# Optimization experiments

Hardware: AMD Instinct MI355X
Metric: run time of the kernel (lower is better)

The kernel has to match this reference:

```python
import jax, jax.numpy as jnp
import numpy as np

TEMPERATURE = 1.0


def setup_inputs() -> dict:
    key = jax.random.key(0)
    k1, k2, k3, k4, k5 = jax.random.split(key, 5)
    B, D, Da, Dv = 8192, 128, 64, 64
    return {
        "a_features": jax.random.normal(k1, (B, D), dtype=jnp.float32),
        "v_features": jax.random.normal(k2, (B, D), dtype=jnp.float32),
        "audio_only_indices": jax.random.randint(k3, (Da,), 0, D, dtype=jnp.int64),
        "image_only_indices": jax.random.randint(k4, (Dv,), 0, D, dtype=jnp.int64),
        "labels": jax.random.randint(k5, (B,), 0, 10, dtype=jnp.int64),
    }


def reference(a_features, v_features, audio_only_indices, image_only_indices, labels):
    # Gather modality-specific feature subspaces: [B, Da] / [B, Dv]
    audio_only = a_features[:, audio_only_indices]          # a-features, audio dims
    image_audio_only = v_features[:, audio_only_indices]    # v-features, audio dims
    image_only = v_features[:, image_only_indices]          # v-features, image dims
    audio_image_only = a_features[:, image_only_indices]    # a-features, image dims

    # Per original: the dot-product partner is detached (stop_gradient).
    # v_loss_i = -log( exp(<v_i, a_i>/T) / sum_j exp(<v_i, a_j>/T) )
    #          = logsumexp_j(S_v[i, j]) - S_v[i, i]
    S_v = jnp.matmul(image_audio_only,
                     jax.lax.stop_gradient(audio_only).T) / TEMPERATURE  # [B, B]
    S_a = jnp.matmul(audio_image_only,
                     jax.lax.stop_gradient(image_only).T) / TEMPERATURE  # [B, B]

    v_loss = jnp.mean(jax.nn.logsumexp(S_v, axis=1) - jnp.diagonal(S_v))
    a_loss = jnp.mean(jax.nn.logsumexp(S_a, axis=1) - jnp.diagonal(S_a))
    return v_loss + a_loss
```

## Files before the change

### kernel.cpp

```cpp
#include <hip/hip_runtime.h>
#include <hip/hip_bf16.h>

typedef __attribute__((ext_vector_type(8))) short bf16x8;
typedef __attribute__((ext_vector_type(4))) float f32x4;

#define BN 8192
#define DF 128
#define DG 64
static constexpr float L2E = 1.44269504088896340736f;
static constexpr float LN2 = 0.69314718055994530942f;

__device__ __forceinline__ size_t frag_off(int row, int d) {
  int tile = row >> 4, m = row & 15;
  int half = d >> 5, q = (d >> 3) & 3, c = d & 7;
  return (size_t)tile * 1024 + (size_t)half * 512 + (size_t)(q * 16 + m) * 8 + c;
}

__global__ __launch_bounds__(256) void gather_k(
    const float* __restrict__ a, const float* __restrict__ v,
    const int* __restrict__ aidx, const int* __restrict__ iidx,
    __hip_bfloat16* __restrict__ Xv, __hip_bfloat16* __restrict__ Ya,
    __hip_bfloat16* __restrict__ Xa, __hip_bfloat16* __restrict__ Yv,
    float* __restrict__ diag, float* __restrict__ rowsum,
    float* __restrict__ out) {
  int tid = threadIdx.x;
  int gid = blockIdx.x * 256 + tid;
  if (gid < 2 * BN) rowsum[gid] = 0.f;
  if (gid == 0) out[0] = 0.f;

  int lane = tid & 63;
  int row  = blockIdx.x * 4 + (tid >> 6);
  int ka = aidx[lane];
  int ki = iidx[lane];

  float2 a2 = ((const float2*)(a + (size_t)row * DF))[lane];
  float2 v2 = ((const float2*)(v + (size_t)row * DF))[lane];

  float axa = __shfl(a2.x, ka >> 1), aya = __shfl(a2.y, ka >> 1);
  float vxa = __shfl(v2.x, ka >> 1), vya = __shfl(v2.y, ka >> 1);
  float axi = __shfl(a2.x, ki >> 1), ayi = __shfl(a2.y, ki >> 1);
  float vxi = __shfl(v2.x, ki >> 1), vyi = __shfl(v2.y, ki >> 1);
  float aa = (ka & 1) ? aya : axa;
  float va = (ka & 1) ? vya : vxa;
  float ai = (ki & 1) ? ayi : axi;
  float vi = (ki & 1) ? vyi : vxi;

  size_t fo = frag_off(row, lane);
  Xv[fo] = __float2bfloat16(va * L2E);
  Ya[fo] = __float2bfloat16(aa);
  Xa[fo] = __float2bfloat16(ai * L2E);
  Yv[fo] = __float2bfloat16(vi);

  float dv = va * aa;
  float da = ai * vi;
#pragma unroll
  for (int off = 32; off >= 1; off >>= 1) {
    dv += __shfl_xor(dv, off);
    da += __shfl_xor(da, off);
  }
  if (lane == 0) {
    diag[row]      = dv;
    diag[BN + row] = da;
  }
}

__global__ __launch_bounds__(256, 8) void lse_main(
    const unsigned short* __restrict__ Xv, const unsigned short* __restrict__ Ya,
    const unsigned short* __restrict__ Xa, const unsigned short* __restrict__ Yv,
    float* __restrict__ rowsum) {
  const unsigned short* X;
  const unsigned short* Y;
  float* rs;
  if (blockIdx.z == 0) { X = Xv; Y = Ya; rs = rowsum; }
  else                 { X = Xa; Y = Yv; rs = rowsum + BN; }

  int tid  = threadIdx.x;
  int lane = tid & 63;
  int m = lane & 15;
  int q = lane >> 4;
  int row0 = blockIdx.x * 128 + (tid >> 6) * 32;

  bf16x8 af[2][2];
#pragma unroll
  for (int t = 0; t < 2; ++t) {
    const unsigned short* p =
        X + (size_t)(row0 / 16 + t) * 1024 + (size_t)lane * 8;
    af[t][0] = *(const bf16x8*)p;
    af[t][1] = *(const bf16x8*)(p + 512);
  }

  f32x4 part[2] = {};
  const f32x4 zero = {0.f, 0.f, 0.f, 0.f};

  const unsigned short* bbase =
      Y + (size_t)(blockIdx.y * 32) * 1024 + (size_t)lane * 8;
  bf16x8 b0 = *(const bf16x8*)bbase;
  bf16x8 b1 = *(const bf16x8*)(bbase + 512);

#define LSE_BODY(B0, B1)                                                      \
  {                                                                           \
    _Pragma("unroll") for (int t = 0; t < 2; ++t) {                           \
      f32x4 c =                                                               \
          __builtin_amdgcn_mfma_f32_16x16x32_bf16(af[t][0], B0, zero, 0, 0, 0); \
      c = __builtin_amdgcn_mfma_f32_16x16x32_bf16(af[t][1], B1, c, 0, 0, 0);  \
      f32x4 e;                                                                \
      e[0] = __builtin_amdgcn_exp2f(c[0]);                                    \
      e[1] = __builtin_amdgcn_exp2f(c[1]);                                    \
      e[2] = __builtin_amdgcn_exp2f(c[2]);                                    \
      e[3] = __builtin_amdgcn_exp2f(c[3]);                                    \
      part[t] += e;                                                           \
    }                                                                         \
  }

  for (int jt = 0; jt < 31; ++jt) {
    const unsigned short* np = bbase + (size_t)(jt + 1) * 1024;
    bf16x8 n0 = *(const bf16x8*)np;
    bf16x8 n1 = *(const bf16x8*)(np + 512);
    LSE_BODY(b0, b1)
    b0 = n0;
    b1 = n1;
  }
  LSE_BODY(b0, b1)
#undef LSE_BODY

#pragma unroll
  for (int off = 1; off < 16; off <<= 1) {
#pragma unroll
    for (int t = 0; t < 2; ++t) {
#pragma unroll
      for (int r = 0; r < 4; ++r)
        part[t][r] += __shfl_xor(part[t][r], off);
    }
  }
  if (m == 0) {
#pragma unroll
    for (int t = 0; t < 2; ++t)
#pragma unroll
      for (int r = 0; r < 4; ++r)
        atomicAdd(&rs[row0 + t * 16 + q * 4 + r], part[t][r]);
  }
}

__global__ __launch_bounds__(256) void finalize_k(
    const float* __restrict__ rowsum, const float* __restrict__ diag,
    float* __restrict__ out) {
  int i = blockIdx.x * 256 + threadIdx.x;
  float local = LN2 * __builtin_amdgcn_logf(rowsum[i]) - diag[i];
#pragma unroll
  for (int off = 32; off >= 1; off >>= 1) local += __shfl_xor(local, off);
  __shared__ float red[4];
  int wave = threadIdx.x >> 6;
  if ((threadIdx.x & 63) == 0) red[wave] = local;
  __syncthreads();
  if (threadIdx.x == 0) {
    float bs = red[0] + red[1] + red[2] + red[3];
    atomicAdd(out, bs * (1.f / (float)BN));
  }
}

extern "C" void kernel_launch(void* const* d_in, const int* in_sizes, int n_in,
                              void* d_out, int out_size, void* d_ws, size_t ws_size,
                              hipStream_t stream) {
  const float* a   = (const float*)d_in[0];
  const float* v   = (const float*)d_in[1];
  const int* aidx  = (const int*)d_in[2];
  const int* iidx  = (const int*)d_in[3];

  char* ws = (char*)d_ws;
  const size_t MB = 1024 * 1024;
  __hip_bfloat16* Xv = (__hip_bfloat16*)(ws + 0 * MB);
  __hip_bfloat16* Ya = (__hip_bfloat16*)(ws + 1 * MB);
  __hip_bfloat16* Xa = (__hip_bfloat16*)(ws + 2 * MB);
  __hip_bfloat16* Yv = (__hip_bfloat16*)(ws + 3 * MB);
  float* diag   = (float*)(ws + 4 * MB);
  float* rowsum = (float*)(ws + 4 * MB + 64 * 1024);

  gather_k<<<BN / 4, 256, 0, stream>>>(a, v, aidx, iidx, Xv, Ya, Xa, Yv,
                                       diag, rowsum, (float*)d_out);
  lse_main<<<dim3(BN / 128, 16, 2), 256, 0, stream>>>(
      (const unsigned short*)Xv, (const unsigned short*)Ya,
      (const unsigned short*)Xa, (const unsigned short*)Yv, rowsum);
  finalize_k<<<64, 256, 0, stream>>>(rowsum, diag, (float*)d_out);
}
```

Before: 93.17 us.

## Switch LSE kernel to 32x32x16 MFMA with ping-pong exp/MFMA overlap

Repacks the bf16 gathered operands into a 32-row fragment layout and has each wave compute 32x32 tiles with mfma_f32_32x32x16_bf16 chains. Two accumulators alternate so one tile's exp2 and accumulation overlap the next tile's MFMA chain, with setprio raised around the MFMAs. The column split is halved (grid y from 16 to 8), so each block covers 1024 columns and there are fewer atomics. The 16-wide accumulators need more registers, so occupancy is capped at 4 blocks per SM instead of 8.

```diff
diff --git a/kernel.cpp b/kernel.cpp
--- a/kernel.cpp
+++ b/kernel.cpp
@@ -3,6 +3,7 @@
 
 typedef __attribute__((ext_vector_type(8))) short bf16x8;
 typedef __attribute__((ext_vector_type(4))) float f32x4;
+typedef __attribute__((ext_vector_type(16))) float f32x16;
 
 #define BN 8192
 #define DF 128
@@ -10,10 +11,11 @@
 static constexpr float L2E = 1.44269504088896340736f;
 static constexpr float LN2 = 0.69314718055994530942f;
 
-__device__ __forceinline__ size_t frag_off(int row, int d) {
-  int tile = row >> 4, m = row & 15;
-  int half = d >> 5, q = (d >> 3) & 3, c = d & 7;
-  return (size_t)tile * 1024 + (size_t)half * 512 + (size_t)(q * 16 + m) * 8 + c;
+__device__ __forceinline__ size_t frag_off32(int row, int d) {
+  int tile = row >> 5;
+  int kk = d >> 4, khi = (d >> 3) & 1, c = d & 7;
+  return (size_t)tile * 2048 + (size_t)kk * 512 +
+         (size_t)(khi * 32 + (row & 31)) * 8 + c;
 }
 
 __global__ __launch_bounds__(256) void gather_k(
@@ -45,7 +47,7 @@
   float ai = (ki & 1) ? ayi : axi;
   float vi = (ki & 1) ? vyi : vxi;
 
-  size_t fo = frag_off(row, lane);
+  size_t fo = frag_off32(row, lane);
   Xv[fo] = __float2bfloat16(va * L2E);
   Ya[fo] = __float2bfloat16(aa);
   Xa[fo] = __float2bfloat16(ai * L2E);
@@ -64,7 +66,7 @@
   }
 }
 
-__global__ __launch_bounds__(256, 8) void lse_main(
+__global__ __launch_bounds__(256, 4) void lse_main(
     const unsigned short* __restrict__ Xv, const unsigned short* __restrict__ Ya,
     const unsigned short* __restrict__ Xa, const unsigned short* __restrict__ Yv,
     float* __restrict__ rowsum) {
@@ -76,68 +78,77 @@
 
   int tid  = threadIdx.x;
   int lane = tid & 63;
-  int m = lane & 15;
-  int q = lane >> 4;
   int row0 = blockIdx.x * 128 + (tid >> 6) * 32;
 
-  bf16x8 af[2][2];
+  const unsigned short* ap =
+      X + (size_t)(row0 >> 5) * 2048 + (size_t)lane * 8;
+  bf16x8 a[4];
 #pragma unroll
-  for (int t = 0; t < 2; ++t) {
-    const unsigned short* p =
-        X + (size_t)(row0 / 16 + t) * 1024 + (size_t)lane * 8;
-    af[t][0] = *(const bf16x8*)p;
-    af[t][1] = *(const bf16x8*)(p + 512);
+  for (int kk = 0; kk < 4; ++kk) a[kk] = *(const bf16x8*)(ap + kk * 512);
+
+  const unsigned short* bbase =
+      Y + (size_t)(blockIdx.y * 32) * 2048 + (size_t)lane * 8;
+
+  const f32x16 zero16 = {};
+  f32x16 part = {};
+  bf16x8 b[4];
+
+#define LOADB(T)                                                              \
+  {                                                                           \
+    const unsigned short* p = bbase + (size_t)(T) * 2048;                     \
+    b[0] = *(const bf16x8*)p;                                                 \
+    b[1] = *(const bf16x8*)(p + 512);                                         \
+    b[2] = *(const bf16x8*)(p + 1024);                                        \
+    b[3] = *(const bf16x8*)(p + 1536);                                        \
+  }
+#define CHAIN(DST)                                                            \
+  {                                                                           \
+    __builtin_amdgcn_s_setprio(1);                                            \
+    DST = __builtin_amdgcn_mfma_f32_32x32x16_bf16(a[0], b[0], zero16, 0, 0, 0); \
+    DST = __builtin_amdgcn_mfma_f32_32x32x16_bf16(a[1], b[1], DST, 0, 0, 0);  \
+    DST = __builtin_amdgcn_mfma_f32_32x32x16_bf16(a[2], b[2], DST, 0, 0, 0);  \
+    DST = __builtin_amdgcn_mfma_f32_32x32x16_bf16(a[3], b[3], DST, 0, 0, 0);  \
+    __builtin_amdgcn_s_setprio(0);                                            \
+  }
+#define EXPACC(C)                                                             \
+  {                                                                           \
+    _Pragma("unroll") for (int r = 0; r < 16; ++r)                            \
+        part[r] += __builtin_amdgcn_exp2f(C[r]);                              \
   }
 
-  f32x4 part[2] = {};
-  const f32x4 zero = {0.f, 0.f, 0.f, 0.f};
-
-  const unsigned short* bbase =
-      Y + (size_t)(blockIdx.y * 32) * 1024 + (size_t)lane * 8;
-  bf16x8 b0 = *(const bf16x8*)bbase;
-  bf16x8 b1 = *(const bf16x8*)(bbase + 512);
-
-#define LSE_BODY(B0, B1)                                                      \
-  {                                                                           \
-    _Pragma("unroll") for (int t = 0; t < 2; ++t) {                           \
-      f32x4 c =                                                               \
-          __builtin_amdgcn_mfma_f32_16x16x32_bf16(af[t][0], B0, zero, 0, 0, 0); \
-      c = __builtin_amdgcn_mfma_f32_16x16x32_bf16(af[t][1], B1, c, 0, 0, 0);  \
-      f32x4 e;                                                                \
-      e[0] = __builtin_amdgcn_exp2f(c[0]);                                    \
-      e[1] = __builtin_amdgcn_exp2f(c[1]);                                    \
-      e[2] = __builtin_amdgcn_exp2f(c[2]);                                    \
-      e[3] = __builtin_amdgcn_exp2f(c[3]);                                    \
-      part[t] += e;                                                           \
-    }                                                                         \
+  f32x16 c0, c1;
+  LOADB(0)
+  CHAIN(c0)
+  LOADB(1)
+  for (int i = 0; i < 15; ++i) {
+    int t = 2 * i + 1;
+    CHAIN(c1)
+    LOADB(t + 1)
+    EXPACC(c0)
+    CHAIN(c0)
+    LOADB(t + 2)
+    EXPACC(c1)
   }
-
-  for (int jt = 0; jt < 31; ++jt) {
-    const unsigned short* np = bbase + (size_t)(jt + 1) * 1024;
-    bf16x8 n0 = *(const bf16x8*)np;
-    bf16x8 n1 = *(const bf16x8*)(np + 512);
-    LSE_BODY(b0, b1)
-    b0 = n0;
-    b1 = n1;
-  }
-  LSE_BODY(b0, b1)
-#undef LSE_BODY
+  CHAIN(c1)
+  EXPACC(c0)
+  EXPACC(c1)
+#undef LOADB
+#undef CHAIN
+#undef EXPACC
 
 #pragma unroll
-  for (int off = 1; off < 16; off <<= 1) {
+  for (int off = 1; off < 32; off <<= 1) {
 #pragma unroll
-    for (int t = 0; t < 2; ++t) {
+    for (int r = 0; r < 16; ++r)
+      part[r] += __shfl_xor(part[r], off);
+  }
+  if ((lane & 31) == 0) {
+    int hi = lane >> 5;
 #pragma unroll
-      for (int r = 0; r < 4; ++r)
-        part[t][r] += __shfl_xor(part[t][r], off);
+    for (int r = 0; r < 16; ++r) {
+      int row = (r & 3) + 8 * (r >> 2) + 4 * hi;
+      atomicAdd(&rs[row0 + row], part[r]);
     }
-  }
-  if (m == 0) {
-#pragma unroll
-    for (int t = 0; t < 2; ++t)
-#pragma unroll
-      for (int r = 0; r < 4; ++r)
-        atomicAdd(&rs[row0 + t * 16 + q * 4 + r], part[t][r]);
   }
 }
 
@@ -177,7 +188,7 @@
 
   gather_k<<<BN / 4, 256, 0, stream>>>(a, v, aidx, iidx, Xv, Ya, Xa, Yv,
                                        diag, rowsum, (float*)d_out);
-  lse_main<<<dim3(BN / 128, 16, 2), 256, 0, stream>>>(
+  lse_main<<<dim3(BN / 128, 8, 2), 256, 0, stream>>>(
       (const unsigned short*)Xv, (const unsigned short*)Ya,
       (const unsigned short*)Xa, (const unsigned short*)Yv, rowsum);
   finalize_k<<<64, 256, 0, stream>>>(rowsum, diag, (float*)d_out);
```

Result: no change. 93.73 us (+0.6%).

## Stage shared B tiles through LDS with async global_load_lds double buffering

Applied to the files above, without the earlier changes.

Before this change, every wave loaded the same B tiles directly from global memory into registers. Now the block cooperatively stages two B tiles per iteration into a double-buffered LDS array using global_load_lds, and all four waves read them from LDS. The goal is to cut redundant global/L2 traffic by a factor of the wave count. In exchange it adds a __syncthreads and a vmcnt wait every iteration, plus LDS read latency.

```diff
diff --git a/kernel.cpp b/kernel.cpp
--- a/kernel.cpp
+++ b/kernel.cpp
@@ -74,11 +74,14 @@
   if (blockIdx.z == 0) { X = Xv; Y = Ya; rs = rowsum; }
   else                 { X = Xa; Y = Yv; rs = rowsum + BN; }
 
+  __shared__ __align__(16) unsigned short sB[2][2048];
+
   int tid  = threadIdx.x;
   int lane = tid & 63;
+  int wid  = tid >> 6;
   int m = lane & 15;
   int q = lane >> 4;
-  int row0 = blockIdx.x * 128 + (tid >> 6) * 32;
+  int row0 = blockIdx.x * 128 + wid * 32;
 
   bf16x8 af[2][2];
 #pragma unroll
@@ -89,39 +92,51 @@
     af[t][1] = *(const bf16x8*)(p + 512);
   }
 
+  const unsigned short* bblock = Y + (size_t)(blockIdx.y * 32) * 1024;
+
+#define STAGE(PAIR, BUF)                                                      \
+  __builtin_amdgcn_global_load_lds(                                           \
+      (const __attribute__((address_space(1))) void*)(                        \
+          bblock + (size_t)(PAIR) * 2048 + wid * 512 + lane * 8),             \
+      (__attribute__((address_space(3))) void*)(                              \
+          &sB[BUF][wid * 512 + lane * 8]),                                    \
+      16, 0, 0);
+
   f32x4 part[2] = {};
   const f32x4 zero = {0.f, 0.f, 0.f, 0.f};
 
-  const unsigned short* bbase =
-      Y + (size_t)(blockIdx.y * 32) * 1024 + (size_t)lane * 8;
-  bf16x8 b0 = *(const bf16x8*)bbase;
-  bf16x8 b1 = *(const bf16x8*)(bbase + 512);
+  STAGE(0, 0)
+  asm volatile("s_waitcnt vmcnt(0)" ::: "memory");
+  __syncthreads();
 
-#define LSE_BODY(B0, B1)                                                      \
-  {                                                                           \
-    _Pragma("unroll") for (int t = 0; t < 2; ++t) {                           \
-      f32x4 c =                                                               \
-          __builtin_amdgcn_mfma_f32_16x16x32_bf16(af[t][0], B0, zero, 0, 0, 0); \
-      c = __builtin_amdgcn_mfma_f32_16x16x32_bf16(af[t][1], B1, c, 0, 0, 0);  \
-      f32x4 e;                                                                \
-      e[0] = __builtin_amdgcn_exp2f(c[0]);                                    \
-      e[1] = __builtin_amdgcn_exp2f(c[1]);                                    \
-      e[2] = __builtin_amdgcn_exp2f(c[2]);                                    \
-      e[3] = __builtin_amdgcn_exp2f(c[3]);                                    \
-      part[t] += e;                                                           \
-    }                                                                         \
+  for (int i = 0; i < 16; ++i) {
+    int cur = i & 1;
+    bf16x8 b[2][2];
+#pragma unroll
+    for (int tt = 0; tt < 2; ++tt) {
+      b[tt][0] = *(const bf16x8*)&sB[cur][tt * 1024 + lane * 8];
+      b[tt][1] = *(const bf16x8*)&sB[cur][tt * 1024 + 512 + lane * 8];
+    }
+    if (i < 15) STAGE(i + 1, cur ^ 1)
+#pragma unroll
+    for (int tt = 0; tt < 2; ++tt) {
+#pragma unroll
+      for (int t = 0; t < 2; ++t) {
+        f32x4 c =
+            __builtin_amdgcn_mfma_f32_16x16x32_bf16(af[t][0], b[tt][0], zero, 0, 0, 0);
+        c = __builtin_amdgcn_mfma_f32_16x16x32_bf16(af[t][1], b[tt][1], c, 0, 0, 0);
+        f32x4 e;
+        e[0] = __builtin_amdgcn_exp2f(c[0]);
+        e[1] = __builtin_amdgcn_exp2f(c[1]);
+        e[2] = __builtin_amdgcn_exp2f(c[2]);
+        e[3] = __builtin_amdgcn_exp2f(c[3]);
+        part[t] += e;
+      }
+    }
+    asm volatile("s_waitcnt vmcnt(0)" ::: "memory");
+    __syncthreads();
   }
-
-  for (int jt = 0; jt < 31; ++jt) {
-    const unsigned short* np = bbase + (size_t)(jt + 1) * 1024;
-    bf16x8 n0 = *(const bf16x8*)np;
-    bf16x8 n1 = *(const bf16x8*)(np + 512);
-    LSE_BODY(b0, b1)
-    b0 = n0;
-    b1 = n1;
-  }
-  LSE_BODY(b0, b1)
-#undef LSE_BODY
+#undef STAGE
 
 #pragma unroll
   for (int off = 1; off < 16; off <<= 1) {
```

Result: no change. 92.23 us (-1.0%).
